# Kernel optimization log

Hardware: AMD Instinct MI355X
Metric: run time of the kernel (lower is better)

## Reference

```python
import jax, jax.numpy as jnp
import numpy as np

N_NODES = 100000
N_EDGES = 800000
IN_DIM, HID_DIM, OUT_DIM = 128, 256, 128


def setup_inputs() -> dict:
    key = jax.random.key(0)
    k1, k2, k3, k4, k5 = jax.random.split(key, 5)
    x = jax.random.normal(k1, (N_NODES, IN_DIM), dtype=jnp.float32)
    edge_index = jax.random.randint(k2, (2, N_EDGES), 0, N_NODES, dtype=jnp.int64)
    edge_weight = jax.random.uniform(k3, (N_EDGES,), dtype=jnp.float32)
    W1 = jax.random.normal(k4, (IN_DIM, HID_DIM), dtype=jnp.float32) * 0.02
    b1 = jnp.zeros((HID_DIM,), dtype=jnp.float32)
    W2 = jax.random.normal(k5, (HID_DIM, OUT_DIM), dtype=jnp.float32) * 0.02
    b2 = jnp.zeros((OUT_DIM,), dtype=jnp.float32)
    return {"x": x, "edge_index": edge_index, "edge_weight": edge_weight,
            "W1": W1, "b1": b1, "W2": W2, "b2": b2}


def reference(x, edge_index, edge_weight, W1, b1, W2, b2):
    # GCNConv (normalize=True, add_self_loops=False), two layers with ReLU.
    # Dropout is identity at inference.
    row = edge_index[0]  # source nodes (E,)
    col = edge_index[1]  # target nodes (E,)
    n = x.shape[0]

    # Symmetric normalization: deg at target, norm = d^-1/2[row]*w*d^-1/2[col]
    deg = jax.ops.segment_sum(edge_weight, col, num_segments=n)  # (N,)
    dis = jnp.where(deg > 0, jax.lax.rsqrt(deg), 0.0)
    norm = dis[row] * edge_weight * dis[col]  # (E,)

    def gcn_conv(h, W, b):
        h = h @ W                                   # (N, F_out)
        msg = h[row] * norm[:, None]                # (E, F_out) gather+scale
        agg = jax.ops.segment_sum(msg, col, num_segments=n)  # scatter-add
        return agg + b

    h = jax.nn.relu(gcn_conv(x.astype(jnp.float32), W1, b1))
    return gcn_conv(h, W2, b2)
```

## Files before the change

kernel.cpp:

```cpp
#include <hip/hip_runtime.h>
#include <hip/hip_bf16.h>
#include <cstdint>
#include <cstddef>

#define N_NODES 100000
#define N_EDGES 800000
#define IN_DIM 128
#define HID_DIM 256
#define OUT_DIM 128

typedef __attribute__((ext_vector_type(8))) short bf16x8;
typedef __attribute__((ext_vector_type(4))) float f32x4;

__device__ __forceinline__ unsigned short f32_to_bf16(float f) {
    __hip_bfloat16 b = __float2bfloat16(f);
    return *reinterpret_cast<unsigned short*>(&b);
}
__device__ __forceinline__ float bf16_lo(uint32_t u) {
    uint32_t v = u << 16; return *reinterpret_cast<float*>(&v);
}
__device__ __forceinline__ float bf16_hi(uint32_t u) {
    uint32_t v = u & 0xffff0000u; return *reinterpret_cast<float*>(&v);
}

__global__ void rank_hist_kernel(const int* __restrict__ ei,
                                 int* __restrict__ cnt,
                                 int* __restrict__ rank) {
    int e = blockIdx.x * 256 + threadIdx.x;
    if (e >= N_EDGES) return;
    rank[e] = atomicAdd(&cnt[ei[N_EDGES + e]], 1);
}

__global__ void scan1_kernel(const int* __restrict__ in, int* __restrict__ out,
                             int* __restrict__ bsums, int n) {
    __shared__ int tmp[256];
    int t = threadIdx.x;
    int i = blockIdx.x * 256 + t;
    int v = (i < n) ? in[i] : 0;
    tmp[t] = v;
    __syncthreads();
    for (int off = 1; off < 256; off <<= 1) {
        int u = (t >= off) ? tmp[t - off] : 0;
        __syncthreads();
        tmp[t] += u;
        __syncthreads();
    }
    if (i < n) out[i] = tmp[t] - v;
    if (t == 255) bsums[blockIdx.x] = tmp[255];
}

__global__ void scan2_kernel(int* __restrict__ bsums, int nb) {
    __shared__ int tmp[512];
    int t = threadIdx.x;
    int v = (t < nb) ? bsums[t] : 0;
    tmp[t] = v;
    __syncthreads();
    for (int off = 1; off < 512; off <<= 1) {
        int u = (t >= off) ? tmp[t - off] : 0;
        __syncthreads();
        tmp[t] += u;
        __syncthreads();
    }
    if (t < nb) bsums[t] = tmp[t] - v;
}

__global__ void scan3_kernel(int* __restrict__ rowp, const int* __restrict__ bsums,
                             int n, int total) {
    int i = blockIdx.x * 256 + threadIdx.x;
    if (i == 0) rowp[n] = total;
    if (i >= n) return;
    rowp[i] += bsums[blockIdx.x];
}

__global__ void place_kernel(const int* __restrict__ ei,
                             const float* __restrict__ ew,
                             const int* __restrict__ rank,
                             const int* __restrict__ rowp,
                             int2* __restrict__ pairs) {
    int e = blockIdx.x * 256 + threadIdx.x;
    if (e >= N_EDGES) return;
    int c = ei[N_EDGES + e];
    int pos = rowp[c] + rank[e];
    pairs[pos] = make_int2(ei[e], __float_as_int(ew[e]));
}

__global__ void deg_dis_kernel(const int* __restrict__ rowp,
                               const int2* __restrict__ pairs,
                               float* __restrict__ dis) {
    int v = blockIdx.x * 256 + threadIdx.x;
    if (v >= N_NODES) return;
    int b = rowp[v], e = rowp[v + 1];
    float d = 0.f;
    for (int j = b; j < e; ++j) d += __int_as_float(pairs[j].y);
    dis[v] = d > 0.f ? rsqrtf(d) : 0.f;
}

__global__ void prep_kernel(const float* __restrict__ x, uint32_t* __restrict__ xb,
                            const float* __restrict__ W1, unsigned short* __restrict__ W1T,
                            const float* __restrict__ W2, unsigned short* __restrict__ W2T) {
    int b = blockIdx.x;
    if (b < 12500) {
        int i = b * 256 + threadIdx.x;
        float4 v = ((const float4*)x)[i];
        uint32_t lo = (uint32_t)f32_to_bf16(v.x) | ((uint32_t)f32_to_bf16(v.y) << 16);
        uint32_t hi = (uint32_t)f32_to_bf16(v.z) | ((uint32_t)f32_to_bf16(v.w) << 16);
        ((uint2*)xb)[i] = make_uint2(lo, hi);
    } else if (b < 12628) {
        int idx = (b - 12500) * 256 + threadIdx.x;
        int r = idx >> 8, c = idx & 255;
        W1T[c * IN_DIM + r] = f32_to_bf16(W1[idx]);
    } else {
        int idx = (b - 12628) * 256 + threadIdx.x;
        int r = idx >> 7, c = idx & 127;
        W2T[c * HID_DIM + r] = f32_to_bf16(W2[idx]);
    }
}

template <bool OUT_BF16>
__global__ void aggregate_kernel(const uint2* __restrict__ feat,
                                 const int* __restrict__ rowp,
                                 const int2* __restrict__ pairs,
                                 const float* __restrict__ dis,
                                 void* __restrict__ out_v,
                                 const float* __restrict__ bias) {
    int gtid = blockIdx.x * blockDim.x + threadIdx.x;
    int node = gtid >> 5;
    int lane = threadIdx.x & 31;
    if (node >= N_NODES) return;
    int beg = rowp[node], end = rowp[node + 1];
    float dv = dis[node];
    float ax = 0.f, ay = 0.f, az = 0.f, aw = 0.f;

    int j = beg;
    for (; j + 4 <= end; j += 4) {
        int2 p[4]; uint2 u[4]; float d[4];
        #pragma unroll
        for (int q = 0; q < 4; ++q) p[q] = pairs[j + q];
        #pragma unroll
        for (int q = 0; q < 4; ++q) {
            u[q] = feat[(size_t)p[q].x * 32 + lane];
            d[q] = dis[p[q].x];
        }
        #pragma unroll
        for (int q = 0; q < 4; ++q) {
            float w = __int_as_float(p[q].y) * d[q] * dv;
            ax += w * bf16_lo(u[q].x); ay += w * bf16_hi(u[q].x);
            az += w * bf16_lo(u[q].y); aw += w * bf16_hi(u[q].y);
        }
    }
    if (j + 2 <= end) {
        int2 p0 = pairs[j], p1 = pairs[j + 1];
        uint2 u0 = feat[(size_t)p0.x * 32 + lane];
        uint2 u1 = feat[(size_t)p1.x * 32 + lane];
        float w0 = __int_as_float(p0.y) * dis[p0.x] * dv;
        float w1 = __int_as_float(p1.y) * dis[p1.x] * dv;
        ax += w0 * bf16_lo(u0.x) + w1 * bf16_lo(u1.x);
        ay += w0 * bf16_hi(u0.x) + w1 * bf16_hi(u1.x);
        az += w0 * bf16_lo(u0.y) + w1 * bf16_lo(u1.y);
        aw += w0 * bf16_hi(u0.y) + w1 * bf16_hi(u1.y);
        j += 2;
    }
    if (j < end) {
        int2 p0 = pairs[j];
        uint2 u0 = feat[(size_t)p0.x * 32 + lane];
        float w0 = __int_as_float(p0.y) * dis[p0.x] * dv;
        ax += w0 * bf16_lo(u0.x); ay += w0 * bf16_hi(u0.x);
        az += w0 * bf16_lo(u0.y); aw += w0 * bf16_hi(u0.y);
    }
    if (bias) {
        float4 b = ((const float4*)bias)[lane];
        ax += b.x; ay += b.y; az += b.z; aw += b.w;
    }
    if (OUT_BF16) {
        uint2 o;
        o.x = (uint32_t)f32_to_bf16(ax) | ((uint32_t)f32_to_bf16(ay) << 16);
        o.y = (uint32_t)f32_to_bf16(az) | ((uint32_t)f32_to_bf16(aw) << 16);
        ((uint2*)out_v)[(size_t)node * 32 + lane] = o;
    } else {
        ((float4*)out_v)[(size_t)node * 32 + lane] = make_float4(ax, ay, az, aw);
    }
}

template <int K, int NC, bool RELU>
__global__ __launch_bounds__(256) void gemm_bf16(const unsigned short* __restrict__ A,
                                                 const unsigned short* __restrict__ BT,
                                                 const float* __restrict__ bias,
                                                 unsigned short* __restrict__ C,
                                                 int M) {
    constexpr int BM = 128, BN = 128, BK = 64;
    __shared__ unsigned short As[BM * BK];
    __shared__ unsigned short Bs[BN * BK];
    int tid = threadIdx.x;
    int wave = tid >> 6, lane = tid & 63;
    int m0 = blockIdx.x * BM, n0 = blockIdx.y * BN;
    int wr = (wave & 1) * 64, wc = (wave >> 1) * 64;
    int fr = lane & 15, fq = lane >> 4;

    f32x4 acc[4][4] = {};

    for (int k0 = 0; k0 < K; k0 += BK) {
        #pragma unroll
        for (int i = 0; i < 4; ++i) {
            int cbase = (i * 4 + wave) * 64;
            int c = cbase + lane;
            int m = c >> 3, qg = (c & 7) ^ (m & 7);
            int gm = m0 + m; if (gm >= M) gm = M - 1;
            const unsigned short* ga = A + (size_t)gm * K + k0 + qg * 8;
            __builtin_amdgcn_global_load_lds(
                (const __attribute__((address_space(1))) void*)ga,
                (__attribute__((address_space(3))) void*)(As + (size_t)cbase * 8),
                16, 0, 0);
            const unsigned short* gb = BT + (size_t)(n0 + m) * K + k0 + qg * 8;
            __builtin_amdgcn_global_load_lds(
                (const __attribute__((address_space(1))) void*)gb,
                (__attribute__((address_space(3))) void*)(Bs + (size_t)cbase * 8),
                16, 0, 0);
        }
        __syncthreads();

        #pragma unroll
        for (int kf = 0; kf < 2; ++kf) {
            int swz = ((kf * 4 + fq) ^ (fr & 7)) * 8;
            bf16x8 af[4], bfr[4];
            #pragma unroll
            for (int mt = 0; mt < 4; ++mt)
                af[mt] = *(const bf16x8*)(As + (wr + mt * 16 + fr) * BK + swz);
            #pragma unroll
            for (int nt = 0; nt < 4; ++nt)
                bfr[nt] = *(const bf16x8*)(Bs + (wc + nt * 16 + fr) * BK + swz);
            #pragma unroll
            for (int mt = 0; mt < 4; ++mt)
                #pragma unroll
                for (int nt = 0; nt < 4; ++nt)
                    acc[mt][nt] = __builtin_amdgcn_mfma_f32_16x16x32_bf16(
                        af[mt], bfr[nt], acc[mt][nt], 0, 0, 0);
        }
        __syncthreads();
    }

    #pragma unroll
    for (int mt = 0; mt < 4; ++mt) {
        #pragma unroll
        for (int r = 0; r < 4; ++r) {
            int row = m0 + wr + mt * 16 + fq * 4 + r;
            if (row >= M) continue;
            #pragma unroll
            for (int nt = 0; nt < 4; ++nt) {
                int col = n0 + wc + nt * 16 + fr;
                float v = acc[mt][nt][r];
                if (bias) v += bias[col];
                if (RELU) v = fmaxf(v, 0.f);
                C[(size_t)row * NC + col] = f32_to_bf16(v);
            }
        }
    }
}

extern "C" void kernel_launch(void* const* d_in, const int* in_sizes, int n_in,
                              void* d_out, int out_size, void* d_ws, size_t ws_size,
                              hipStream_t stream) {
    const float* x  = (const float*)d_in[0];
    const int*   ei = (const int*)d_in[1];
    const float* ew = (const float*)d_in[2];
    const float* W1 = (const float*)d_in[3];
    const float* b1 = (const float*)d_in[4];
    const float* W2 = (const float*)d_in[5];
    const float* b2 = (const float*)d_in[6];
    float* out = (float*)d_out;

    char* ws = (char*)d_ws;
    size_t off = 0;
    auto alloc = [&](size_t bytes) -> void* {
        void* p = ws + off;
        off = (off + bytes + 255) & ~(size_t)255;
        return p;
    };
    int*   cnt   = (int*)  alloc((size_t)N_NODES * 4);
    float* dis   = (float*)alloc((size_t)N_NODES * 4);
    int*   rowp  = (int*)  alloc((size_t)(N_NODES + 1) * 4);
    int*   bsums = (int*)  alloc(512 * 4);
    int*   rank  = (int*)  alloc((size_t)N_EDGES * 4);
    int2*  pairs = (int2*) alloc((size_t)N_EDGES * 8);
    uint32_t* xb = (uint32_t*)alloc((size_t)N_NODES * IN_DIM * 2);
    unsigned short* W1T = (unsigned short*)alloc((size_t)IN_DIM * HID_DIM * 2);
    unsigned short* W2T = (unsigned short*)alloc((size_t)HID_DIM * OUT_DIM * 2);
    unsigned short* A1  = (unsigned short*)alloc((size_t)N_NODES * IN_DIM * 2);
    unsigned short* h1  = (unsigned short*)alloc((size_t)N_NODES * HID_DIM * 2);

    hipMemsetAsync(cnt, 0, (size_t)N_NODES * 4, stream);

    int ne_blocks = (N_EDGES + 255) / 256;
    int nn_blocks = (N_NODES + 255) / 256;

    rank_hist_kernel<<<ne_blocks, 256, 0, stream>>>(ei, cnt, rank);
    scan1_kernel<<<nn_blocks, 256, 0, stream>>>(cnt, rowp, bsums, N_NODES);
    scan2_kernel<<<1, 512, 0, stream>>>(bsums, nn_blocks);
    scan3_kernel<<<nn_blocks, 256, 0, stream>>>(rowp, bsums, N_NODES, N_EDGES);
    place_kernel<<<ne_blocks, 256, 0, stream>>>(ei, ew, rank, rowp, pairs);
    deg_dis_kernel<<<nn_blocks, 256, 0, stream>>>(rowp, pairs, dis);
    prep_kernel<<<12756, 256, 0, stream>>>(x, xb, W1, W1T, W2, W2T);

    int agg_blocks = (N_NODES * 32) / 256;

    aggregate_kernel<true><<<agg_blocks, 256, 0, stream>>>(
        (const uint2*)xb, rowp, pairs, dis, A1, nullptr);
    dim3 g1((N_NODES + 127) / 128, HID_DIM / 128);
    gemm_bf16<IN_DIM, HID_DIM, true><<<g1, 256, 0, stream>>>(A1, W1T, b1, h1, N_NODES);

    unsigned short* t = A1;
    dim3 g2((N_NODES + 127) / 128, OUT_DIM / 128);
    gemm_bf16<HID_DIM, OUT_DIM, false><<<g2, 256, 0, stream>>>(h1, W2T, nullptr, t, N_NODES);
    aggregate_kernel<false><<<agg_blocks, 256, 0, stream>>>(
        (const uint2*)t, rowp, pairs, dis, out, b2);
}
```

Baseline: 316.8 us.

## Fuse both dense GEMMs into one kernel keeping hidden tile in LDS

Replaces the two separate bf16 GEMM launches (A1·W1 with bias+ReLU into h1, then h1·W2) with one kernel. Each 128-row block computes the 256-wide hidden layer in two 128-column halves, stages each half in LDS, and immediately accumulates its contribution to the 128-wide output. This removes writing and re-reading the N×256 bf16 hidden tensor from global memory plus one launch. Weight fragments are now read straight from global/L2 instead of LDS, and the larger LDS footprint (about 67 KB) may reduce occupancy.

Measured after the change: 297.9 us. 1.06x faster.

```diff
diff --git a/kernel.cpp b/kernel.cpp
--- a/kernel.cpp
+++ b/kernel.cpp
@@ -181,79 +181,104 @@
     }
 }
 
-template <int K, int NC, bool RELU>
-__global__ __launch_bounds__(256) void gemm_bf16(const unsigned short* __restrict__ A,
-                                                 const unsigned short* __restrict__ BT,
-                                                 const float* __restrict__ bias,
-                                                 unsigned short* __restrict__ C,
-                                                 int M) {
-    constexpr int BM = 128, BN = 128, BK = 64;
-    __shared__ unsigned short As[BM * BK];
-    __shared__ unsigned short Bs[BN * BK];
+__global__ __launch_bounds__(256) void gemm_fused_kernel(
+    const unsigned short* __restrict__ A,
+    const unsigned short* __restrict__ W1T,
+    const float* __restrict__ b1,
+    const unsigned short* __restrict__ W2T,
+    unsigned short* __restrict__ T,
+    int M) {
+    __shared__ unsigned short As[128 * 128];
+    __shared__ unsigned short Hs[128 * 136];
     int tid = threadIdx.x;
     int wave = tid >> 6, lane = tid & 63;
-    int m0 = blockIdx.x * BM, n0 = blockIdx.y * BN;
+    int m0 = blockIdx.x * 128;
     int wr = (wave & 1) * 64, wc = (wave >> 1) * 64;
     int fr = lane & 15, fq = lane >> 4;
 
-    f32x4 acc[4][4] = {};
-
-    for (int k0 = 0; k0 < K; k0 += BK) {
-        #pragma unroll
-        for (int i = 0; i < 4; ++i) {
-            int cbase = (i * 4 + wave) * 64;
-            int c = cbase + lane;
-            int m = c >> 3, qg = (c & 7) ^ (m & 7);
-            int gm = m0 + m; if (gm >= M) gm = M - 1;
-            const unsigned short* ga = A + (size_t)gm * K + k0 + qg * 8;
-            __builtin_amdgcn_global_load_lds(
-                (const __attribute__((address_space(1))) void*)ga,
-                (__attribute__((address_space(3))) void*)(As + (size_t)cbase * 8),
-                16, 0, 0);
-            const unsigned short* gb = BT + (size_t)(n0 + m) * K + k0 + qg * 8;
-            __builtin_amdgcn_global_load_lds(
-                (const __attribute__((address_space(1))) void*)gb,
-                (__attribute__((address_space(3))) void*)(Bs + (size_t)cbase * 8),
-                16, 0, 0);
-        }
-        __syncthreads();
-
-        #pragma unroll
-        for (int kf = 0; kf < 2; ++kf) {
-            int swz = ((kf * 4 + fq) ^ (fr & 7)) * 8;
-            bf16x8 af[4], bfr[4];
+    #pragma unroll
+    for (int i = 0; i < 8; ++i) {
+        int cbase = (i * 4 + wave) * 64;
+        int c = cbase + lane;
+        int m = c >> 4, cl = c & 15;
+        int qg = ((cl & 7) ^ (m & 7)) | (cl & 8);
+        int gm = m0 + m; if (gm >= M) gm = M - 1;
+        const unsigned short* ga = A + (size_t)gm * 128 + qg * 8;
+        __builtin_amdgcn_global_load_lds(
+            (const __attribute__((address_space(1))) void*)ga,
+            (__attribute__((address_space(3))) void*)(As + (size_t)cbase * 8),
+            16, 0, 0);
+    }
+    __syncthreads();
+
+    f32x4 acc_t[4][4] = {};
+    #pragma unroll
+    for (int nh = 0; nh < 2; ++nh) {
+        f32x4 acc_h[4][4] = {};
+        #pragma unroll
+        for (int ks = 0; ks < 4; ++ks) {
+            int q = ks * 4 + fq;
+            int cl = ((q & 7) ^ (fr & 7)) | (q & 8);
+            bf16x8 af[4], wf[4];
             #pragma unroll
             for (int mt = 0; mt < 4; ++mt)
-                af[mt] = *(const bf16x8*)(As + (wr + mt * 16 + fr) * BK + swz);
+                af[mt] = *(const bf16x8*)(As + (wr + mt * 16 + fr) * 128 + cl * 8);
             #pragma unroll
             for (int nt = 0; nt < 4; ++nt)
-                bfr[nt] = *(const bf16x8*)(Bs + (wc + nt * 16 + fr) * BK + swz);
+                wf[nt] = *(const bf16x8*)(W1T +
+                    (size_t)(nh * 128 + wc + nt * 16 + fr) * 128 + ks * 32 + fq * 8);
             #pragma unroll
             for (int mt = 0; mt < 4; ++mt)
                 #pragma unroll
                 for (int nt = 0; nt < 4; ++nt)
-                    acc[mt][nt] = __builtin_amdgcn_mfma_f32_16x16x32_bf16(
-                        af[mt], bfr[nt], acc[mt][nt], 0, 0, 0);
-        }
-        __syncthreads();
+                    acc_h[mt][nt] = __builtin_amdgcn_mfma_f32_16x16x32_bf16(
+                        af[mt], wf[nt], acc_h[mt][nt], 0, 0, 0);
+        }
+        float bv[4];
+        #pragma unroll
+        for (int nt = 0; nt < 4; ++nt) bv[nt] = b1[nh * 128 + wc + nt * 16 + fr];
+        __syncthreads();
+        #pragma unroll
+        for (int mt = 0; mt < 4; ++mt)
+            #pragma unroll
+            for (int r = 0; r < 4; ++r) {
+                int row = wr + mt * 16 + fq * 4 + r;
+                #pragma unroll
+                for (int nt = 0; nt < 4; ++nt) {
+                    float v = fmaxf(acc_h[mt][nt][r] + bv[nt], 0.f);
+                    Hs[row * 136 + wc + nt * 16 + fr] = f32_to_bf16(v);
+                }
+            }
+        __syncthreads();
+        #pragma unroll
+        for (int ks = 0; ks < 4; ++ks) {
+            bf16x8 hf[4], wf[4];
+            #pragma unroll
+            for (int mt = 0; mt < 4; ++mt)
+                hf[mt] = *(const bf16x8*)(Hs + (wr + mt * 16 + fr) * 136 + ks * 32 + fq * 8);
+            #pragma unroll
+            for (int nt = 0; nt < 4; ++nt)
+                wf[nt] = *(const bf16x8*)(W2T +
+                    (size_t)(wc + nt * 16 + fr) * 256 + nh * 128 + ks * 32 + fq * 8);
+            #pragma unroll
+            for (int mt = 0; mt < 4; ++mt)
+                #pragma unroll
+                for (int nt = 0; nt < 4; ++nt)
+                    acc_t[mt][nt] = __builtin_amdgcn_mfma_f32_16x16x32_bf16(
+                        hf[mt], wf[nt], acc_t[mt][nt], 0, 0, 0);
+        }
     }
 
     #pragma unroll
-    for (int mt = 0; mt < 4; ++mt) {
+    for (int mt = 0; mt < 4; ++mt)
         #pragma unroll
         for (int r = 0; r < 4; ++r) {
             int row = m0 + wr + mt * 16 + fq * 4 + r;
             if (row >= M) continue;
             #pragma unroll
-            for (int nt = 0; nt < 4; ++nt) {
-                int col = n0 + wc + nt * 16 + fr;
-                float v = acc[mt][nt][r];
-                if (bias) v += bias[col];
-                if (RELU) v = fmaxf(v, 0.f);
-                C[(size_t)row * NC + col] = f32_to_bf16(v);
-            }
-        }
-    }
+            for (int nt = 0; nt < 4; ++nt)
+                T[(size_t)row * 128 + wc + nt * 16 + fr] = f32_to_bf16(acc_t[mt][nt][r]);
+        }
 }
 
 extern "C" void kernel_launch(void* const* d_in, const int* in_sizes, int n_in,
@@ -285,7 +310,7 @@
     unsigned short* W1T = (unsigned short*)alloc((size_t)IN_DIM * HID_DIM * 2);
     unsigned short* W2T = (unsigned short*)alloc((size_t)HID_DIM * OUT_DIM * 2);
     unsigned short* A1  = (unsigned short*)alloc((size_t)N_NODES * IN_DIM * 2);
-    unsigned short* h1  = (unsigned short*)alloc((size_t)N_NODES * HID_DIM * 2);
+    unsigned short* t   = (unsigned short*)alloc((size_t)N_NODES * OUT_DIM * 2);
 
     hipMemsetAsync(cnt, 0, (size_t)N_NODES * 4, stream);
 
@@ -304,12 +329,10 @@
 
     aggregate_kernel<true><<<agg_blocks, 256, 0, stream>>>(
         (const uint2*)xb, rowp, pairs, dis, A1, nullptr);
-    dim3 g1((N_NODES + 127) / 128, HID_DIM / 128);
-    gemm_bf16<IN_DIM, HID_DIM, true><<<g1, 256, 0, stream>>>(A1, W1T, b1, h1, N_NODES);
-
-    unsigned short* t = A1;
-    dim3 g2((N_NODES + 127) / 128, OUT_DIM / 128);
-    gemm_bf16<HID_DIM, OUT_DIM, false><<<g2, 256, 0, stream>>>(h1, W2T, nullptr, t, N_NODES);
+
+    gemm_fused_kernel<<<(N_NODES + 127) / 128, 256, 0, stream>>>(
+        A1, W1T, b1, W2T, t, N_NODES);
+
     aggregate_kernel<false><<<agg_blocks, 256, 0, stream>>>(
         (const uint2*)t, rowp, pairs, dis, out, b2);
 }
```
